# Kernel optimization log

Hardware: AMD Instinct MI355X
Metric: run time of the kernel (lower is better)

Reference implementation:

```python
import jax, jax.numpy as jnp
import numpy as np

EOS_IDX = 2
B, S, T = 512, 64, 32
V, E, H, DENC, L = 128, 256, 512, 1024, 2


def setup_inputs() -> dict:
    key = jax.random.key(0)
    ks = jax.random.split(key, 24)
    s = 0.02
    inp = {
        "encoder_out": jax.random.normal(ks[0], (B, S, DENC), jnp.float32),
        "h0": jax.random.normal(ks[1], (L, B, H), jnp.float32),
        "c0": jax.random.normal(ks[2], (L, B, H), jnp.float32),
        "targets": jax.random.randint(ks[3], (B, T), 0, V),
        "mask": jax.random.randint(ks[4], (B, S), 0, 2).astype(jnp.int32),
        # parameters
        "emb": jax.random.normal(ks[5], (V, E), jnp.float32) * s,
        "W_enc": jax.random.normal(ks[6], (H, DENC), jnp.float32) * s,
        "W_dec": jax.random.normal(ks[7], (H, H), jnp.float32) * s,
        "v": jax.random.normal(ks[8], (H,), jnp.float32) * s,
        "W_ih0": jax.random.normal(ks[9], (4 * H, E + DENC), jnp.float32) * s,
        "W_hh0": jax.random.normal(ks[10], (4 * H, H), jnp.float32) * s,
        "b_ih0": jax.random.normal(ks[11], (4 * H,), jnp.float32) * s,
        "b_hh0": jax.random.normal(ks[12], (4 * H,), jnp.float32) * s,
        "W_ih1": jax.random.normal(ks[13], (4 * H, H), jnp.float32) * s,
        "W_hh1": jax.random.normal(ks[14], (4 * H, H), jnp.float32) * s,
        "b_ih1": jax.random.normal(ks[15], (4 * H,), jnp.float32) * s,
        "b_hh1": jax.random.normal(ks[16], (4 * H,), jnp.float32) * s,
        "W_out": jax.random.normal(ks[17], (V, H + DENC + E), jnp.float32) * s,
        "b_out": jax.random.normal(ks[18], (V,), jnp.float32) * s,
    }
    # guarantee at least one valid source position per row
    inp["mask"] = inp["mask"].at[:, 0].set(1)
    return inp


def _lstm_cell(x, h, c, W_ih, W_hh, b_ih, b_hh):
    gates = x @ W_ih.T + b_ih + h @ W_hh.T + b_hh  # (B, 4H)
    i, f, g, o = jnp.split(gates, 4, axis=-1)      # torch gate order i,f,g,o
    c_new = jax.nn.sigmoid(f) * c + jax.nn.sigmoid(i) * jnp.tanh(g)
    h_new = jax.nn.sigmoid(o) * jnp.tanh(c_new)
    return h_new, c_new


def reference(encoder_out, h0, c0, targets, mask,
              emb, W_enc, W_dec, v,
              W_ih0, W_hh0, b_ih0, b_hh0,
              W_ih1, W_hh1, b_ih1, b_hh1,
              W_out, b_out):
    # teacher_forcing_ratio = 1.0: input tokens are [EOS, targets[:, :-1]]
    tokens = jnp.concatenate(
        [jnp.full((targets.shape[0], 1), EOS_IDX, dtype=targets.dtype),
         targets[:, :-1]], axis=1)                       # (B, T)
    embedded = emb[tokens]                               # (B, T, E)
    enc_proj = jnp.einsum('bsd,hd->bsh', encoder_out, W_enc)  # precompute W_enc(encoder_out)
    mask_b = mask > 0                                    # (B, S)

    def step(carry, x_emb):                              # x_emb: (B, E)
        h, c = carry                                     # each (L, B, H)
        h_top = h[-1]                                    # (B, H)
        dec_proj = h_top @ W_dec.T                       # (B, H)
        energy = jnp.tanh(dec_proj[:, None, :] + enc_proj)   # (B, S, H)
        score = jnp.einsum('bsh,h->bs', energy, v)       # (B, S)
        score = jnp.where(mask_b, score, -jnp.inf)
        weights = jax.nn.softmax(score, axis=-1)         # (B, S)
        context = jnp.einsum('bs,bsd->bd', weights, encoder_out)  # (B, DENC)
        x = jnp.concatenate([x_emb, context], axis=-1)   # (B, E+DENC)
        h0n, c0n = _lstm_cell(x, h[0], c[0], W_ih0, W_hh0, b_ih0, b_hh0)
        h1n, c1n = _lstm_cell(h0n, h[1], c[1], W_ih1, W_hh1, b_ih1, b_hh1)
        pred = jnp.concatenate([h1n, context, x_emb], axis=-1) @ W_out.T + b_out  # (B, V)
        return (jnp.stack([h0n, h1n]), jnp.stack([c0n, c1n])), pred

    (_, _), preds = jax.lax.scan(step, (h0, c0), jnp.swapaxes(embedded, 0, 1))
    return jnp.swapaxes(preds, 0, 1)                     # (B, T, V)
```

## Files before the change

### kernel.cpp

```cpp
#include <hip/hip_runtime.h>
#include <math.h>

#define BB 512
#define SS 64
#define TT 32
#define VV 128
#define EE 256
#define HH 512
#define DENC 1024
#define BH (BB*HH)
#define XW0 1792
#define XW1 1024
#define PW  1792
#define G4H 2048

typedef __attribute__((ext_vector_type(8))) short bf16x8;
typedef __attribute__((ext_vector_type(4))) short bf16x4;
typedef __attribute__((ext_vector_type(4))) float f32x4;

__device__ __forceinline__ float sigf(float x){ return 1.f/(1.f+expf(-x)); }
__device__ __forceinline__ float bf2f(short s){
  return __uint_as_float(((unsigned)(unsigned short)s) << 16);
}
__device__ __forceinline__ short f2bf(float f){
  unsigned u = __float_as_uint(f);
  return (short)((u + 0x7FFF + ((u>>16)&1)) >> 16);
}
__device__ __forceinline__ float tanh_fast(float x){
  x = fminf(fmaxf(x, -15.f), 15.f);
  float e = __expf(2.f*x);
  return (e - 1.f) / (e + 1.f);
}

__device__ __forceinline__ void zacc(f32x4 a[2][2]){
  #pragma unroll
  for (int i = 0; i < 2; ++i)
    #pragma unroll
    for (int j = 0; j < 2; ++j) a[i][j] = {0.f,0.f,0.f,0.f};
}

template<int BM, int BN>
struct GemmPipe {
  static constexpr int LA = 72;
  static __device__ __forceinline__ void run(short* Asb, short* Bsb,
      const short* __restrict__ A, const short* __restrict__ Bt,
      int lda, int ldb, int kBase, int nIter,
      int rowBase, int colBase, int tid, f32x4 acc[BM/32][BN/32])
  {
    constexpr int FI = BM/32, FJ = BN/32, ACH = BM/32, BCH = BN/32;
    const int lane = tid & 63, wave = tid >> 6;
    const int ml = lane & 15, kq = lane >> 4;
    const int wm = (wave >> 1)*(BM/2), wn = (wave & 1)*(BN/2);
    const int arow = (tid*ACH) >> 3, acol = ((tid*ACH) & 7)*8;
    const int brow = (tid*BCH) >> 3, bcol = ((tid*BCH) & 7)*8;
    const short* Ap = A + (size_t)(rowBase+arow)*lda + kBase + acol;
    const short* Bp = Bt + (size_t)(colBase+brow)*ldb + kBase + bcol;
    bf16x8 ar[ACH], br[BCH];
    #pragma unroll
    for (int c = 0; c < ACH; ++c) ar[c] = *(const bf16x8*)(Ap + c*8);
    #pragma unroll
    for (int c = 0; c < BCH; ++c) br[c] = *(const bf16x8*)(Bp + c*8);
    for (int i = 0; i < nIter; ++i) {
      short* Ab = Asb + (i&1)*(BM*LA);
      short* Bb = Bsb + (i&1)*(BN*LA);
      #pragma unroll
      for (int c = 0; c < ACH; ++c) *(bf16x8*)&Ab[arow*LA + acol + c*8] = ar[c];
      #pragma unroll
      for (int c = 0; c < BCH; ++c) *(bf16x8*)&Bb[brow*LA + bcol + c*8] = br[c];
      __syncthreads();
      if (i+1 < nIter) {
        const short* An = Ap + (size_t)(i+1)*64;
        const short* Bn = Bp + (size_t)(i+1)*64;
        #pragma unroll
        for (int c = 0; c < ACH; ++c) ar[c] = *(const bf16x8*)(An + c*8);
        #pragma unroll
        for (int c = 0; c < BCH; ++c) br[c] = *(const bf16x8*)(Bn + c*8);
      }
      #pragma unroll
      for (int kh = 0; kh < 2; ++kh) {
        bf16x8 af[FI], bfv[FJ];
        #pragma unroll
        for (int ii = 0; ii < FI; ++ii)
          af[ii] = *(const bf16x8*)&Ab[(wm + ii*16 + ml)*LA + kh*32 + kq*8];
        #pragma unroll
        for (int jj = 0; jj < FJ; ++jj)
          bfv[jj] = *(const bf16x8*)&Bb[(wn + jj*16 + ml)*LA + kh*32 + kq*8];
        #pragma unroll
        for (int ii = 0; ii < FI; ++ii)
          #pragma unroll
          for (int jj = 0; jj < FJ; ++jj)
            acc[ii][jj] = __builtin_amdgcn_mfma_f32_16x16x32_bf16(af[ii], bfv[jj], acc[ii][jj], 0,0,0);
      }
    }
    __syncthreads();
  }
};


__device__ __forceinline__ void attn_role(int aid, int tid, char* smem, int t,
    const short* __restrict__ enc_proj, const short* __restrict__ enc_out,
    const float* __restrict__ vvec, const int* __restrict__ mask,
    const int* __restrict__ targets, const short* __restrict__ embb,
    const short* __restrict__ hb, const short* __restrict__ wdecT,
    short* __restrict__ xcat0, short* __restrict__ predcat)
{
  const int b0 = aid*2;
  float* hbf = (float*)smem;
  float* dps = (float*)(smem + 4096);
  float* vvf = (float*)(smem + 12288);
  float* sc  = (float*)(smem + 14336);
  float* wt  = (float*)(smem + 14848);
  {
    bf16x4 h4 = *(const bf16x4*)&hb[(size_t)b0*HH + tid*4];
    #pragma unroll
    for (int j = 0; j < 4; ++j) hbf[tid*4 + j] = bf2f(h4[j]);
    vvf[tid] = vvec[tid];
    vvf[256 + tid] = vvec[256 + tid];
  }
  __syncthreads();
  {
    int unit = tid & 127, ksel = tid >> 7;
    int bb = unit >> 6, h8 = unit & 63;
    const short* wp = wdecT + (size_t)(ksel*256)*HH + h8*8;
    const float* hrow = hbf + bb*HH + ksel*256;
    float a[8] = {0.f,0.f,0.f,0.f,0.f,0.f,0.f,0.f};
    for (int k = 0; k < 256; ++k) {
      bf16x8 w8 = *(const bf16x8*)(wp + (size_t)k*HH);
      float x = hrow[k];
      #pragma unroll
      for (int j = 0; j < 8; ++j) a[j] += x * bf2f(w8[j]);
    }
    float* d = dps + (ksel*2 + bb)*HH + h8*8;
    #pragma unroll
    for (int j = 0; j < 8; ++j) d[j] = a[j];
  }
  __syncthreads();
  {
    int bb = tid >> 7, h0_ = (tid & 127)*4;
    f32x4 s0 = *(f32x4*)&dps[bb*HH + h0_];
    f32x4 s1 = *(f32x4*)&dps[(2 + bb)*HH + h0_];
    *(f32x4*)&dps[bb*HH + h0_] = s0 + s1;
  }
  __syncthreads();
  {
    int u = tid >> 1, khalf = tid & 1;
    int bb = u >> 6, s = u & 63;
    const short* ep = enc_proj + ((size_t)(b0+bb)*SS + s)*HH + khalf*256;
    const float* dpp = dps + bb*HH + khalf*256;
    const float* vp  = vvf + khalf*256;
    float accv = 0.f;
    for (int hc = 0; hc < 32; ++hc) {
      bf16x8 e8 = *(const bf16x8*)(ep + hc*8);
      f32x4 d0 = *(const f32x4*)(dpp + hc*8);
      f32x4 d1 = *(const f32x4*)(dpp + hc*8 + 4);
      f32x4 v0 = *(const f32x4*)(vp + hc*8);
      f32x4 v1 = *(const f32x4*)(vp + hc*8 + 4);
      #pragma unroll
      for (int j = 0; j < 4; ++j) accv += v0[j]*tanh_fast(d0[j] + bf2f(e8[j]));
      #pragma unroll
      for (int j = 0; j < 4; ++j) accv += v1[j]*tanh_fast(d1[j] + bf2f(e8[4+j]));
    }
    accv += __shfl_xor(accv, 1, 64);
    if (khalf == 0) sc[bb*64 + s] = accv;
  }
  __syncthreads();
  if (tid < 128) {
    int bb = tid >> 6, s = tid & 63;
    int valid = mask[(b0+bb)*SS + s];
    float x = valid ? sc[bb*64 + s] : -INFINITY;
    float mx = x;
    #pragma unroll
    for (int off = 32; off; off >>= 1) mx = fmaxf(mx, __shfl_xor(mx, off, 64));
    float e = valid ? __expf(x - mx) : 0.f;
    float sum = e;
    #pragma unroll
    for (int off = 32; off; off >>= 1) sum += __shfl_xor(sum, off, 64);
    wt[bb*64 + s] = e / sum;
  }
  __syncthreads();
  {
    int bb = tid >> 7, d0 = (tid & 127)*8;
    const short* eob = enc_out + (size_t)(b0+bb)*SS*DENC + d0;
    float ca[8] = {0.f,0.f,0.f,0.f,0.f,0.f,0.f,0.f};
    for (int s = 0; s < SS; ++s) {
      float w = wt[bb*64 + s];
      bf16x8 e8 = *(const bf16x8*)(eob + (size_t)s*DENC);
      #pragma unroll
      for (int j = 0; j < 8; ++j) ca[j] += w * bf2f(e8[j]);
    }
    bf16x8 cb8;
    #pragma unroll
    for (int j = 0; j < 8; ++j) cb8[j] = f2bf(ca[j]);
    int b_ = b0 + bb;
    *(bf16x8*)&xcat0[(size_t)b_*XW0 + EE + d0] = cb8;
    *(bf16x8*)&predcat[(size_t)b_*PW + HH + d0] = cb8;
  }
  #pragma unroll
  for (int bb = 0; bb < 2; ++bb) {
    int b_ = b0 + bb;
    int tok = (t == 0) ? 2 : targets[b_*TT + t - 1];
    predcat[(size_t)b_*PW + HH + DENC + tid] = embb[tok*EE + tid];
  }
}

__device__ __forceinline__ void out_role(int idx, int tid, char* smem,
    const short* __restrict__ predprev, const short* __restrict__ wout,
    const float* __restrict__ b_out, float* __restrict__ out, int t)
{
  short* As = (short*)smem;
  short* Bs = (short*)(smem + 18432);
  const int rowBase = (idx >> 1)*64, colBase = (idx & 1)*64;
  f32x4 acc[2][2];
  zacc(acc);
  GemmPipe<64,64>::run(As, Bs, predprev, wout, PW, PW, 0, PW/64, rowBase, colBase, tid, acc);
  const int lane = tid & 63, wave = tid >> 6, ml = lane & 15, kq = lane >> 4;
  const int wm = (wave >> 1)*32, wn = (wave & 1)*32;
  #pragma unroll
  for (int ii = 0; ii < 2; ++ii)
    #pragma unroll
    for (int jj = 0; jj < 2; ++jj) {
      int n = colBase + wn + jj*16 + ml;
      float bv = b_out[n];
      #pragma unroll
      for (int r2 = 0; r2 < 4; ++r2) {
        int m = rowBase + wm + ii*16 + kq*4 + r2;
        out[(size_t)m*(TT*VV) + (size_t)(t-1)*VV + n] = acc[ii][jj][r2] + bv;
      }
    }
}

__device__ __forceinline__ void pstore(int tid, int rowBase, int colBase,
    float* __restrict__ P, f32x4 acc[2][2])
{
  const int lane = tid & 63, wave = tid >> 6, ml = lane & 15, kq = lane >> 4;
  const int wm = (wave >> 1)*32, wn = (wave & 1)*32;
  #pragma unroll
  for (int ii = 0; ii < 2; ++ii)
    #pragma unroll
    for (int jj = 0; jj < 2; ++jj)
      #pragma unroll
      for (int r2 = 0; r2 < 4; ++r2)
        P[(size_t)(rowBase + wm + ii*16 + kq*4 + r2)*G4H + colBase + wn + jj*16 + ml] = acc[ii][jj][r2];
}

template<int BM>
__device__ __forceinline__ void gates_epi(int tid, int rowBase, int colBase,
    char* smem, f32x4 acc[BM/32][2], const float* __restrict__ bias,
    float* __restrict__ cb,
    short* __restrict__ d1, int ld1, short* __restrict__ d2, int ld2,
    short* __restrict__ d3)
{
  const int lane = tid & 63, wave = tid >> 6, ml = lane & 15, kq = lane >> 4;
  const int wm = (wave >> 1)*(BM/2), wn = (wave & 1)*32;
  float* Ct = (float*)smem;
  float bj0 = bias[colBase + wn + ml];
  float bj1 = bias[colBase + wn + 16 + ml];
  #pragma unroll
  for (int ii = 0; ii < BM/32; ++ii)
    #pragma unroll
    for (int jj = 0; jj < 2; ++jj)
      #pragma unroll
      for (int r2 = 0; r2 < 4; ++r2)
        Ct[(wm + ii*16 + kq*4 + r2)*68 + wn + jj*16 + ml] = acc[ii][jj][r2] + (jj ? bj1 : bj0);
  __syncthreads();
  #pragma unroll
  for (int kk = 0; kk < BM/16; ++kk) {
    int cidx = tid + kk*256;
    int m = cidx >> 4, hl = cidx & 15;
    float4 gv = *(float4*)&Ct[m*68 + hl*4];
    int b_ = rowBase + m, h_ = (colBase >> 2) + hl;
    float cp = cb[b_*HH + h_];
    float cn = sigf(gv.y)*cp + sigf(gv.x)*tanhf(gv.z);
    float hn = sigf(gv.w)*tanhf(cn);
    cb[b_*HH + h_] = cn;
    short hb16 = f2bf(hn);
    d1[(size_t)b_*ld1 + h_] = hb16;
    d2[(size_t)b_*ld2 + h_] = hb16;
    if (d3) d3[(size_t)b_*HH + h_] = hb16;
  }
}

__device__ __forceinline__ void emb_prewrite(int rowBase, int tid,
    short* __restrict__ xc0n, const int* __restrict__ targets,
    const short* __restrict__ embb, int t)
{
  int b_ = rowBase + (tid >> 2);
  int tok = targets[b_*TT + t];
  const short* src = embb + tok*EE + (tid & 3)*64;
  short* dst = xc0n + (size_t)b_*XW0 + (tid & 3)*64;
  #pragma unroll
  for (int j = 0; j < 8; ++j)
    *(bf16x8*)(dst + j*8) = *(const bf16x8*)(src + j*8);
}


__global__ __launch_bounds__(256)
void attn_pg01(const short* __restrict__ enc_proj, const short* __restrict__ enc_out,
               const float* __restrict__ vvec, const int* __restrict__ mask,
               const int* __restrict__ targets, const short* __restrict__ embb,
               const short* __restrict__ hb, const short* __restrict__ wdecT,
               short* __restrict__ xcat0, short* __restrict__ predcat,
               const short* __restrict__ wcat0, float* __restrict__ P0,
               const short* __restrict__ xcat1, const short* __restrict__ wcat1,
               float* __restrict__ P1,
               const short* __restrict__ predprev, const short* __restrict__ wout,
               float* __restrict__ Pout, int t)
{
  __shared__ __align__(16) char smem[36864];
  const int tid = threadIdx.x, bid = blockIdx.x;
  if (bid < 256) {
    attn_role(bid, tid, smem, t, enc_proj, enc_out, vvec, mask, targets,
              embb, hb, wdecT, xcat0, predcat);
  } else if (bid < 512) {
    short* As = (short*)smem;
    short* Bs = (short*)(smem + 18432);
    int idx = bid - 256;
    int rowBase = (idx >> 5)*64, colBase = (idx & 31)*64;
    f32x4 acc[2][2];
    zacc(acc);
    GemmPipe<64,64>::run(As, Bs, xcat0, wcat0, XW0, XW0, 0,    4, rowBase, colBase, tid, acc);
    GemmPipe<64,64>::run(As, Bs, xcat0, wcat0, XW0, XW0, 1280, 8, rowBase, colBase, tid, acc);
    pstore(tid, rowBase, colBase, P0, acc);
  } else if (bid < 768) {
    short* As = (short*)smem;
    short* Bs = (short*)(smem + 18432);
    int idx = bid - 512;
    int rowBase = (idx >> 5)*64, colBase = (idx & 31)*64;
    f32x4 acc[2][2];
    zacc(acc);
    GemmPipe<64,64>::run(As, Bs, xcat1, wcat1, XW1, XW1, 512, 8, rowBase, colBase, tid, acc);
    pstore(tid, rowBase, colBase, P1, acc);
  } else {
    if (t >= 1) {
      short* As = (short*)smem;
      short* Bs = (short*)(smem + 18432);
      int idx = bid - 768;
      int q = idx >> 4, oIdx = idx & 15;
      int rowBase = (oIdx >> 1)*64, colBase = (oIdx & 1)*64;
      f32x4 acc[2][2];
      zacc(acc);
      GemmPipe<64,64>::run(As, Bs, predprev, wout, PW, PW, q*448, 7,
                           rowBase, colBase, tid, acc);
      const int lane = tid & 63, wave = tid >> 6, ml = lane & 15, kq = lane >> 4;
      const int wm = (wave >> 1)*32, wn = (wave & 1)*32;
      float* Pt = Pout + q*65536;
      #pragma unroll
      for (int ii = 0; ii < 2; ++ii)
        #pragma unroll
        for (int jj = 0; jj < 2; ++jj)
          #pragma unroll
          for (int r2 = 0; r2 < 4; ++r2)
            Pt[(rowBase + wm + ii*16 + kq*4 + r2)*VV + colBase + wn + jj*16 + ml] = acc[ii][jj][r2];
    }
  }
}

__global__ __launch_bounds__(256)
void gates0_fin(const short* __restrict__ A, const short* __restrict__ W,
                const float* __restrict__ bias, const float* __restrict__ P0,
                float* __restrict__ cb,
                short* __restrict__ d1, short* __restrict__ d2,
                short* __restrict__ xc0n, const int* __restrict__ targets,
                const short* __restrict__ embb,
                const float* __restrict__ Pout, const float* __restrict__ b_out,
                float* __restrict__ out, int t)
{
  __shared__ __align__(16) char smem[27648];
  const int tid = threadIdx.x, bid = blockIdx.x;
  if (bid >= 520) {
    if (t >= 1) {
      int base = (bid - 520)*8192 + tid*32;
      #pragma unroll
      for (int j = 0; j < 8; ++j) {
        int i = base + j*4;
        f32x4 a = *(const f32x4*)&Pout[i];
        f32x4 b = *(const f32x4*)&Pout[65536 + i];
        f32x4 c = *(const f32x4*)&Pout[131072 + i];
        f32x4 d = *(const f32x4*)&Pout[196608 + i];
        int m = i >> 7, n = i & 127;
        f32x4 bo = *(const f32x4*)&b_out[n];
        f32x4 r = a + b + c + d + bo;
        *(f32x4*)&out[(size_t)m*(TT*VV) + (size_t)(t-1)*VV + n] = r;
      }
    }
    return;
  }
  if (bid >= 512) {
    if (t + 1 < TT) emb_prewrite((bid - 512)*64, tid, xc0n, targets, embb, t);
    return;
  }
  short* As = (short*)smem;
  short* Bs = (short*)(smem + 9216);
  const int rowBase = (bid >> 5)*32, colBase = (bid & 31)*64;
  const int lane = tid & 63, wave = tid >> 6, ml = lane & 15, kq = lane >> 4;
  const int wm = (wave >> 1)*16, wn = (wave & 1)*32;
  f32x4 acc[1][2];
  const float* Pp = P0 + (size_t)rowBase*G4H + colBase;
  #pragma unroll
  for (int jj = 0; jj < 2; ++jj)
    #pragma unroll
    for (int r2 = 0; r2 < 4; ++r2)
      acc[0][jj][r2] = Pp[(wm + kq*4 + r2)*G4H + wn + jj*16 + ml];
  GemmPipe<32,64>::run(As, Bs, A, W, XW0, XW0, 256, 16, rowBase, colBase, tid, acc);
  gates_epi<32>(tid, rowBase, colBase, smem, acc, bias, cb, d1, XW1, d2, XW0, (short*)nullptr);
}

__global__ __launch_bounds__(256)
void gates1_fin(const short* __restrict__ A, const short* __restrict__ W,
                const float* __restrict__ bias, const float* __restrict__ P1,
                float* __restrict__ cb,
                short* __restrict__ d1, short* __restrict__ d2, short* __restrict__ d3)
{
  __shared__ __align__(16) char smem[27648];
  const int tid = threadIdx.x, bid = blockIdx.x;
  short* As = (short*)smem;
  short* Bs = (short*)(smem + 9216);
  const int rowBase = (bid >> 5)*32, colBase = (bid & 31)*64;
  const int lane = tid & 63, wave = tid >> 6, ml = lane & 15, kq = lane >> 4;
  const int wm = (wave >> 1)*16, wn = (wave & 1)*32;
  f32x4 acc[1][2];
  const float* Pp = P1 + (size_t)rowBase*G4H + colBase;
  #pragma unroll
  for (int jj = 0; jj < 2; ++jj)
    #pragma unroll
    for (int r2 = 0; r2 < 4; ++r2)
      acc[0][jj][r2] = Pp[(wm + kq*4 + r2)*G4H + wn + jj*16 + ml];
  GemmPipe<32,64>::run(As, Bs, A, W, XW1, XW1, 0, 8, rowBase, colBase, tid, acc);
  gates_epi<32>(tid, rowBase, colBase, smem, acc, bias, cb, d1, XW1, d2, PW, d3);
}

__global__ __launch_bounds__(256)
void out_fin(const short* __restrict__ predprev, const short* __restrict__ wout,
             const float* __restrict__ b_out, float* __restrict__ out)
{
  __shared__ __align__(16) char smem[36864];
  out_role(blockIdx.x, threadIdx.x, smem, predprev, wout, b_out, out, TT);
}

__global__ __launch_bounds__(256)
void enc_gemm(short* __restrict__ C, const short* __restrict__ A, const short* __restrict__ Bt,
              int K, int ldc)
{
  __shared__ __align__(16) char smem[55296];
  short* As = (short*)smem;
  short* Bs = (short*)(smem + 18432);
  const int tid = threadIdx.x;
  const int rowBase = blockIdx.y*64, colBase = blockIdx.x*128;
  f32x4 acc[2][4];
  #pragma unroll
  for (int i = 0; i < 2; ++i)
    #pragma unroll
    for (int j = 0; j < 4; ++j) acc[i][j] = {0.f,0.f,0.f,0.f};
  GemmPipe<64,128>::run(As, Bs, A, Bt, K, K, 0, K >> 6, rowBase, colBase, tid, acc);
  const int lane = tid & 63, wave = tid >> 6, ml = lane & 15, kq = lane >> 4;
  const int wm = (wave >> 1)*32, wn = (wave & 1)*64;
  #pragma unroll
  for (int ii = 0; ii < 2; ++ii)
    #pragma unroll
    for (int jj = 0; jj < 4; ++jj) {
      int n = colBase + wn + jj*16 + ml;
      #pragma unroll
      for (int r2 = 0; r2 < 4; ++r2) {
        int m = rowBase + wm + ii*16 + kq*4 + r2;
        C[(size_t)m*ldc + n] = f2bf(acc[ii][jj][r2]);
      }
    }
}

__global__ __launch_bounds__(256)
void build_wcat_bf(short* __restrict__ wcat0, short* __restrict__ wcat1,
                   const float* __restrict__ wih0, const float* __restrict__ whh0,
                   const float* __restrict__ wih1, const float* __restrict__ whh1)
{
  int idx = blockIdx.x*256 + threadIdx.x;
  const int N0 = G4H*XW0;
  if (idx < N0) {
    int n = idx / XW0, k = idx % XW0;
    int row = (n & 3)*HH + (n >> 2);
    float v = (k < EE+DENC) ? wih0[(size_t)row*(EE+DENC) + k] : whh0[(size_t)row*HH + (k - (EE+DENC))];
    wcat0[idx] = f2bf(v);
  } else {
    int j = idx - N0;
    int n = j / XW1, k = j % XW1;
    int row = (n & 3)*HH + (n >> 2);
    float v = (k < HH) ? wih1[(size_t)row*HH + k] : whh1[(size_t)row*HH + (k - HH)];
    wcat1[j] = f2bf(v);
  }
}

__global__ __launch_bounds__(256)
void cvt_encout(short* __restrict__ dst, const float* __restrict__ src)
{
  size_t i8 = ((size_t)blockIdx.x*256 + threadIdx.x)*8;
  float4 a = *(const float4*)&src[i8];
  float4 b = *(const float4*)&src[i8+4];
  bf16x8 o;
  o[0]=f2bf(a.x); o[1]=f2bf(a.y); o[2]=f2bf(a.z); o[3]=f2bf(a.w);
  o[4]=f2bf(b.x); o[5]=f2bf(b.y); o[6]=f2bf(b.z); o[7]=f2bf(b.w);
  *(bf16x8*)&dst[i8] = o;
}

__global__ __launch_bounds__(256)
void prep_misc(float* __restrict__ cbuf, short* __restrict__ xcat0a, short* __restrict__ xcat1a,
               short* __restrict__ hb, short* __restrict__ wdecT, short* __restrict__ wenc,
               short* __restrict__ wout, short* __restrict__ embb,
               float* __restrict__ bias0i, float* __restrict__ bias1i,
               const float* __restrict__ c0, const float* __restrict__ h0,
               const float* __restrict__ W_dec, const float* __restrict__ W_enc,
               const float* __restrict__ W_out, const float* __restrict__ emb,
               const float* __restrict__ b_ih0, const float* __restrict__ b_hh0,
               const float* __restrict__ b_ih1, const float* __restrict__ b_hh1)
{
  int idx = blockIdx.x*256 + threadIdx.x;
  if (idx < 524288) { cbuf[idx] = c0[idx]; return; }
  idx -= 524288;
  if (idx < 262144) {
    int b = idx >> 9, h = idx & 511;
    xcat0a[(size_t)b*XW0 + EE + DENC + h] = f2bf(h0[idx]);
    return;
  }
  idx -= 262144;
  if (idx < 262144) {
    int b = idx >> 9, h = idx & 511;
    short v = f2bf(h0[BH + idx]);
    xcat1a[(size_t)b*XW1 + HH + h] = v;
    hb[idx] = v;
    return;
  }
  idx -= 262144;
  if (idx < 262144) {
    int k = idx >> 9, n = idx & 511;
    wdecT[idx] = f2bf(W_dec[(size_t)n*HH + k]);
    return;
  }
  idx -= 262144;
  if (idx < 524288) { wenc[idx] = f2bf(W_enc[idx]); return; }
  idx -= 524288;
  if (idx < 229376) { wout[idx] = f2bf(W_out[idx]); return; }
  idx -= 229376;
  if (idx < 32768)  { embb[idx] = f2bf(emb[idx]); return; }
  idx -= 32768;
  if (idx < 2048) {
    int row = (idx & 3)*HH + (idx >> 2);
    bias0i[idx] = b_ih0[row] + b_hh0[row];
    return;
  }
  idx -= 2048;
  if (idx < 2048) {
    int row = (idx & 3)*HH + (idx >> 2);
    bias1i[idx] = b_ih1[row] + b_hh1[row];
    return;
  }
  idx -= 2048;
  {
    int b = idx >> 8, e = idx & 255;
    xcat0a[(size_t)b*XW0 + e] = f2bf(emb[2*EE + e]);
  }
}

extern "C" void kernel_launch(void* const* d_in, const int* in_sizes, int n_in,
                              void* d_out, int out_size, void* d_ws, size_t ws_size,
                              hipStream_t stream) {
  const float* enc_out = (const float*)d_in[0];
  const float* h0      = (const float*)d_in[1];
  const float* c0      = (const float*)d_in[2];
  const int*   targets = (const int*)d_in[3];
  const int*   mask    = (const int*)d_in[4];
  const float* emb     = (const float*)d_in[5];
  const float* W_enc   = (const float*)d_in[6];
  const float* W_dec   = (const float*)d_in[7];
  const float* v       = (const float*)d_in[8];
  const float* b_ih0   = (const float*)d_in[11];
  const float* b_hh0   = (const float*)d_in[12];
  const float* b_ih1   = (const float*)d_in[15];
  const float* b_hh1   = (const float*)d_in[16];
  const float* b_out   = (const float*)d_in[18];
  float* out = (float*)d_out;

  char* ws = (char*)d_ws;
  size_t o = 0;
  short* enc_out_bf = (short*)(ws + o); o += (size_t)BB*SS*DENC*2;
  short* enc_proj_bf= (short*)(ws + o); o += (size_t)BB*SS*HH*2;
  short* wcat0i     = (short*)(ws + o); o += (size_t)G4H*XW0*2;
  short* wcat1i     = (short*)(ws + o); o += (size_t)G4H*XW1*2;
  short* wdecT      = (short*)(ws + o); o += (size_t)HH*HH*2;
  short* wenc_bf    = (short*)(ws + o); o += (size_t)HH*DENC*2;
  short* wout_bf    = (short*)(ws + o); o += (size_t)VV*PW*2;
  short* emb_bf     = (short*)(ws + o); o += (size_t)VV*EE*2;
  short* xcat0a     = (short*)(ws + o); o += (size_t)BB*XW0*2;
  short* xcat0b     = (short*)(ws + o); o += (size_t)BB*XW0*2;
  short* xcat1a     = (short*)(ws + o); o += (size_t)BB*XW1*2;
  short* xcat1b     = (short*)(ws + o); o += (size_t)BB*XW1*2;
  short* predcata   = (short*)(ws + o); o += (size_t)BB*PW*2;
  short* predcatb   = (short*)(ws + o); o += (size_t)BB*PW*2;
  short* hb         = (short*)(ws + o); o += (size_t)BH*2;
  float* cbuf       = (float*)(ws + o); o += (size_t)2*BH*4;
  float* bias0i     = (float*)(ws + o); o += (size_t)G4H*4;
  float* bias1i     = (float*)(ws + o); o += (size_t)G4H*4;
  float* P0         = (float*)(ws + o); o += (size_t)BB*G4H*4;
  float* P1         = (float*)(ws + o); o += (size_t)BB*G4H*4;
  float* Pout       = (float*)(ws + o); o += (size_t)4*BB*VV*4;
  (void)ws_size; (void)in_sizes; (void)n_in; (void)out_size;

  cvt_encout<<<16384, 256, 0, stream>>>(enc_out_bf, enc_out);
  build_wcat_bf<<<22528, 256, 0, stream>>>(wcat0i, wcat1i,
      (const float*)d_in[9], (const float*)d_in[10], (const float*)d_in[13], (const float*)d_in[14]);
  prep_misc<<<8720, 256, 0, stream>>>(cbuf, xcat0a, xcat1a, hb, wdecT, wenc_bf, wout_bf, emb_bf,
      bias0i, bias1i, c0, h0, W_dec, W_enc, (const float*)d_in[17], emb,
      b_ih0, b_hh0, b_ih1, b_hh1);
  enc_gemm<<<dim3(HH/128, (BB*SS)/64), 256, 0, stream>>>(
      enc_proj_bf, enc_out_bf, wenc_bf, DENC, HH);

  short* xc0[2] = {xcat0a, xcat0b};
  short* xc1[2] = {xcat1a, xcat1b};
  short* pc[2]  = {predcata, predcatb};
  for (int t = 0; t < TT; ++t) {
    attn_pg01<<<832, 256, 0, stream>>>(enc_proj_bf, enc_out_bf, v, mask, targets, emb_bf,
        hb, wdecT, xc0[t&1], pc[t&1], wcat0i, P0, xc1[t&1], wcat1i, P1,
        pc[(t+1)&1], wout_bf, Pout, t);
    gates0_fin<<<528, 256, 0, stream>>>(
        xc0[t&1], wcat0i, bias0i, P0, cbuf, xc1[t&1], xc0[(t+1)&1] + EE + DENC,
        xc0[(t+1)&1], targets, emb_bf, Pout, b_out, out, t);
    gates1_fin<<<512, 256, 0, stream>>>(
        xc1[t&1], wcat1i, bias1i, P1, cbuf + BH, xc1[(t+1)&1] + HH, pc[t&1], hb);
  }
  out_fin<<<16, 256, 0, stream>>>(pc[1], wout_bf, b_out, out);
}
```

Baseline: 2.654 ms.

## Move next-step layer-0 partial gate GEMM into gates1 kernel; split W_dec matvec four ways

The layer-0 partial GEMM over the embedding and h0 columns for step t+1 now runs inside the gates1 launch of step t, in 512 extra blocks. Only t=0 computes it in attn_pg01, which shrinks that kernel's per-step grid. The attention W_dec matvec now splits K four ways with 16 outputs per thread, using more shared memory and a 4-way reduction. This moves work off the critical attention kernel and into one that runs alongside the layer-1 finisher. The trade-off is a larger gates1 grid and a new dependency on h0 written earlier by gates0_fin.

```diff
diff --git a/kernel.cpp b/kernel.cpp
--- a/kernel.cpp
+++ b/kernel.cpp
@@ -107,9 +107,9 @@
   const int b0 = aid*2;
   float* hbf = (float*)smem;
   float* dps = (float*)(smem + 4096);
-  float* vvf = (float*)(smem + 12288);
-  float* sc  = (float*)(smem + 14336);
-  float* wt  = (float*)(smem + 14848);
+  float* vvf = (float*)(smem + 20480);
+  float* sc  = (float*)(smem + 22528);
+  float* wt  = (float*)(smem + 23040);
   {
     bf16x4 h4 = *(const bf16x4*)&hb[(size_t)b0*HH + tid*4];
     #pragma unroll
@@ -119,27 +119,34 @@
   }
   __syncthreads();
   {
-    int unit = tid & 127, ksel = tid >> 7;
-    int bb = unit >> 6, h8 = unit & 63;
-    const short* wp = wdecT + (size_t)(ksel*256)*HH + h8*8;
-    const float* hrow = hbf + bb*HH + ksel*256;
-    float a[8] = {0.f,0.f,0.f,0.f,0.f,0.f,0.f,0.f};
-    for (int k = 0; k < 256; ++k) {
-      bf16x8 w8 = *(const bf16x8*)(wp + (size_t)k*HH);
+    int unit = tid & 63, kq4 = tid >> 6;
+    int bb = unit >> 5, h16 = unit & 31;
+    const short* wp = wdecT + (size_t)(kq4*128)*HH + h16*16;
+    const float* hrow = hbf + bb*HH + kq4*128;
+    float a[16];
+    #pragma unroll
+    for (int j = 0; j < 16; ++j) a[j] = 0.f;
+    for (int k = 0; k < 128; ++k) {
+      bf16x8 w0 = *(const bf16x8*)(wp + (size_t)k*HH);
+      bf16x8 w1 = *(const bf16x8*)(wp + (size_t)k*HH + 8);
       float x = hrow[k];
       #pragma unroll
-      for (int j = 0; j < 8; ++j) a[j] += x * bf2f(w8[j]);
-    }
-    float* d = dps + (ksel*2 + bb)*HH + h8*8;
-    #pragma unroll
-    for (int j = 0; j < 8; ++j) d[j] = a[j];
+      for (int j = 0; j < 8; ++j) a[j] += x * bf2f(w0[j]);
+      #pragma unroll
+      for (int j = 0; j < 8; ++j) a[8+j] += x * bf2f(w1[j]);
+    }
+    float* d = dps + (kq4*2 + bb)*HH + h16*16;
+    #pragma unroll
+    for (int j = 0; j < 16; ++j) d[j] = a[j];
   }
   __syncthreads();
   {
     int bb = tid >> 7, h0_ = (tid & 127)*4;
-    f32x4 s0 = *(f32x4*)&dps[bb*HH + h0_];
+    f32x4 s0 = *(f32x4*)&dps[(0 + bb)*HH + h0_];
     f32x4 s1 = *(f32x4*)&dps[(2 + bb)*HH + h0_];
-    *(f32x4*)&dps[bb*HH + h0_] = s0 + s1;
+    f32x4 s2 = *(f32x4*)&dps[(4 + bb)*HH + h0_];
+    f32x4 s3 = *(f32x4*)&dps[(6 + bb)*HH + h0_];
+    *(f32x4*)&dps[bb*HH + h0_] = (s0 + s1) + (s2 + s3);
   }
   __syncthreads();
   {
@@ -243,6 +250,18 @@
         P[(size_t)(rowBase + wm + ii*16 + kq*4 + r2)*G4H + colBase + wn + jj*16 + ml] = acc[ii][jj][r2];
 }
 
+__device__ __forceinline__ void pstore32(int tid, int rowBase, int colBase,
+    float* __restrict__ P, f32x4 acc[1][2])
+{
+  const int lane = tid & 63, wave = tid >> 6, ml = lane & 15, kq = lane >> 4;
+  const int wm = (wave >> 1)*16, wn = (wave & 1)*32;
+  #pragma unroll
+  for (int jj = 0; jj < 2; ++jj)
+    #pragma unroll
+    for (int r2 = 0; r2 < 4; ++r2)
+      P[(size_t)(rowBase + wm + kq*4 + r2)*G4H + colBase + wn + jj*16 + ml] = acc[0][jj][r2];
+}
+
 template<int BM>
 __device__ __forceinline__ void gates_epi(int tid, int rowBase, int colBase,
     char* smem, f32x4 acc[BM/32][2], const float* __restrict__ bias,
@@ -318,23 +337,13 @@
     int rowBase = (idx >> 5)*64, colBase = (idx & 31)*64;
     f32x4 acc[2][2];
     zacc(acc);
-    GemmPipe<64,64>::run(As, Bs, xcat0, wcat0, XW0, XW0, 0,    4, rowBase, colBase, tid, acc);
-    GemmPipe<64,64>::run(As, Bs, xcat0, wcat0, XW0, XW0, 1280, 8, rowBase, colBase, tid, acc);
-    pstore(tid, rowBase, colBase, P0, acc);
-  } else if (bid < 768) {
-    short* As = (short*)smem;
-    short* Bs = (short*)(smem + 18432);
-    int idx = bid - 512;
-    int rowBase = (idx >> 5)*64, colBase = (idx & 31)*64;
-    f32x4 acc[2][2];
-    zacc(acc);
     GemmPipe<64,64>::run(As, Bs, xcat1, wcat1, XW1, XW1, 512, 8, rowBase, colBase, tid, acc);
     pstore(tid, rowBase, colBase, P1, acc);
-  } else {
+  } else if (bid < 576) {
     if (t >= 1) {
       short* As = (short*)smem;
       short* Bs = (short*)(smem + 18432);
-      int idx = bid - 768;
+      int idx = bid - 512;
       int q = idx >> 4, oIdx = idx & 15;
       int rowBase = (oIdx >> 1)*64, colBase = (oIdx & 1)*64;
       f32x4 acc[2][2];
@@ -351,6 +360,18 @@
           #pragma unroll
           for (int r2 = 0; r2 < 4; ++r2)
             Pt[(rowBase + wm + ii*16 + kq*4 + r2)*VV + colBase + wn + jj*16 + ml] = acc[ii][jj][r2];
+    }
+  } else {
+    if (t == 0) {
+      short* As = (short*)smem;
+      short* Bs = (short*)(smem + 18432);
+      int idx = bid - 576;
+      int rowBase = (idx >> 5)*64, colBase = (idx & 31)*64;
+      f32x4 acc[2][2];
+      zacc(acc);
+      GemmPipe<64,64>::run(As, Bs, xcat0, wcat0, XW0, XW0, 0,    4, rowBase, colBase, tid, acc);
+      GemmPipe<64,64>::run(As, Bs, xcat0, wcat0, XW0, XW0, 1280, 8, rowBase, colBase, tid, acc);
+      pstore(tid, rowBase, colBase, P0, acc);
     }
   }
 }
@@ -406,13 +427,30 @@
 }
 
 __global__ __launch_bounds__(256)
-void gates1_fin(const short* __restrict__ A, const short* __restrict__ W,
+void gates1_pg0(const short* __restrict__ A, const short* __restrict__ W,
                 const float* __restrict__ bias, const float* __restrict__ P1,
                 float* __restrict__ cb,
-                short* __restrict__ d1, short* __restrict__ d2, short* __restrict__ d3)
+                short* __restrict__ d1, short* __restrict__ d2, short* __restrict__ d3,
+                const short* __restrict__ xc0n, const short* __restrict__ wcat0,
+                float* __restrict__ P0, int t)
 {
   __shared__ __align__(16) char smem[27648];
   const int tid = threadIdx.x, bid = blockIdx.x;
+  if (bid >= 512) {
+    if (t + 1 < TT) {
+      short* As = (short*)smem;
+      short* Bs = (short*)(smem + 9216);
+      int idx = bid - 512;
+      int rowBase = (idx >> 5)*32, colBase = (idx & 31)*64;
+      f32x4 acc[1][2];
+      #pragma unroll
+      for (int jj = 0; jj < 2; ++jj) acc[0][jj] = {0.f,0.f,0.f,0.f};
+      GemmPipe<32,64>::run(As, Bs, xc0n, wcat0, XW0, XW0, 0,    4, rowBase, colBase, tid, acc);
+      GemmPipe<32,64>::run(As, Bs, xc0n, wcat0, XW0, XW0, 1280, 8, rowBase, colBase, tid, acc);
+      pstore32(tid, rowBase, colBase, P0, acc);
+    }
+    return;
+  }
   short* As = (short*)smem;
   short* Bs = (short*)(smem + 9216);
   const int rowBase = (bid >> 5)*32, colBase = (bid & 31)*64;
@@ -621,8 +659,9 @@
     gates0_fin<<<528, 256, 0, stream>>>(
         xc0[t&1], wcat0i, bias0i, P0, cbuf, xc1[t&1], xc0[(t+1)&1] + EE + DENC,
         xc0[(t+1)&1], targets, emb_bf, Pout, b_out, out, t);
-    gates1_fin<<<512, 256, 0, stream>>>(
-        xc1[t&1], wcat1i, bias1i, P1, cbuf + BH, xc1[(t+1)&1] + HH, pc[t&1], hb);
+    gates1_pg0<<<1024, 256, 0, stream>>>(
+        xc1[t&1], wcat1i, bias1i, P1, cbuf + BH, xc1[(t+1)&1] + HH, pc[t&1], hb,
+        xc0[(t+1)&1], wcat0i, P0, t);
   }
   out_fin<<<16, 256, 0, stream>>>(pc[1], wout_bf, b_out, out);
 }
```

Result: faster. 2.478 ms (-6.6%).
